# Performance work log

Measured on AMD Instinct MI355X. Metric: run time of the kernel, lower is better.

Reference implementation:

```python
import jax, jax.numpy as jnp
import numpy as np

B, N, K, C = 8, 4096, 16, 128
HID, DEPTH = 4 * C, 2
EPS = 1e-5


def _bn(x, g, b, m, v):
    # BatchNorm1d in eval mode over the last (channel) dim
    return (x - m) * (g * jax.lax.rsqrt(v + EPS)) + b


def _ffn(x, w1, b1, w2, b2, g, bt, m, v):
    h = jax.nn.relu(jnp.einsum('bnc,ch->bnh', x, w1) + b1)
    y = jnp.einsum('bnh,hc->bnc', h, w2) + b2
    return _bn(y, g, bt, m, v)


def setup_inputs() -> dict:
    key = jax.random.key(0)
    ks = jax.random.split(key, 24)
    s = 0.05
    inp = {
        'x': jax.random.normal(ks[0], (B, N, C), jnp.float32),
        'knn_idx': jax.random.randint(ks[1], (B, N, K), 0, N, jnp.int64),
        'mlp0_w1': jax.random.normal(ks[2], (C, HID), jnp.float32) * s,
        'mlp0_b1': jax.random.normal(ks[3], (HID,), jnp.float32) * s,
        'mlp0_w2': jax.random.normal(ks[4], (HID, C), jnp.float32) * s,
        'mlp0_b2': jax.random.normal(ks[5], (C,), jnp.float32) * s,
        'mlp0_g': jax.random.uniform(ks[6], (C,), jnp.float32, 0.5, 1.5),
        'mlp0_beta': jax.random.normal(ks[7], (C,), jnp.float32) * s,
        'mlp0_m': jnp.zeros((C,), jnp.float32),
        'mlp0_v': jnp.ones((C,), jnp.float32),
        'vfr_w': jax.random.normal(ks[8], (DEPTH, C, C), jnp.float32) * s,
        'vfr_b': jax.random.normal(ks[9], (DEPTH, C), jnp.float32) * s,
        'vfr_g': jax.random.uniform(ks[10], (DEPTH, C), jnp.float32, 0.5, 1.5),
        'vfr_beta': jax.random.normal(ks[11], (DEPTH, C), jnp.float32) * s,
        'vfr_m': jnp.zeros((DEPTH, C), jnp.float32),
        'vfr_v': jnp.ones((DEPTH, C), jnp.float32),
        'ffn_w1': jax.random.normal(ks[12], (DEPTH, C, HID), jnp.float32) * s,
        'ffn_b1': jax.random.normal(ks[13], (DEPTH, HID), jnp.float32) * s,
        'ffn_w2': jax.random.normal(ks[14], (DEPTH, HID, C), jnp.float32) * s,
        'ffn_b2': jax.random.normal(ks[15], (DEPTH, C), jnp.float32) * s,
        'ffn_g': jax.random.uniform(ks[16], (DEPTH, C), jnp.float32, 0.5, 1.5),
        'ffn_beta': jax.random.normal(ks[17], (DEPTH, C), jnp.float32) * s,
        'ffn_m': jnp.zeros((DEPTH, C), jnp.float32),
        'ffn_v': jnp.ones((DEPTH, C), jnp.float32),
    }
    return inp


def reference(x, knn_idx,
              mlp0_w1, mlp0_b1, mlp0_w2, mlp0_b2, mlp0_g, mlp0_beta, mlp0_m, mlp0_v,
              vfr_w, vfr_b, vfr_g, vfr_beta, vfr_m, vfr_v,
              ffn_w1, ffn_b1, ffn_w2, ffn_b2, ffn_g, ffn_beta, ffn_m, ffn_v):
    # eval mode: DropPath is identity, BatchNorm uses running stats
    x = x + _ffn(x, mlp0_w1, mlp0_b1, mlp0_w2, mlp0_b2, mlp0_g, mlp0_beta, mlp0_m, mlp0_v)
    gather = jax.vmap(lambda pts, idx: pts[idx])  # [N,C],[N,K] -> [N,K,C]
    for i in range(DEPTH):
        # VFR: linear -> knn gather -> edge diff -> max over K -> BN
        h = jnp.einsum('bnc,cd->bnd', x, vfr_w[i]) + vfr_b[i]
        nb = gather(h, knn_idx)                      # [B,N,K,C]
        agg = jnp.max(nb - h[:, :, None, :], axis=2)  # [B,N,C]
        x = x + _bn(agg, vfr_g[i], vfr_beta[i], vfr_m[i], vfr_v[i])
        x = x + _ffn(x, ffn_w1[i], ffn_b1[i], ffn_w2[i], ffn_b2[i],
                     ffn_g[i], ffn_beta[i], ffn_m[i], ffn_v[i])
    return x
```

## Files before the change

### kernel.cpp

```cpp
#include <hip/hip_runtime.h>
#include <hip/hip_bf16.h>
#include <stdint.h>

typedef __attribute__((ext_vector_type(8))) __bf16 bf16x8;
typedef __attribute__((ext_vector_type(4))) float floatx4;

#define EPS 1e-5f

__device__ __forceinline__ unsigned short f2bf(float f) {
    union { float f; unsigned int u; } x; x.f = f;
    unsigned int r = x.u + 0x7fffu + ((x.u >> 16) & 1u);
    return (unsigned short)(r >> 16);
}
__device__ __forceinline__ float bf2f_lo(unsigned int u) {
    union { unsigned int u; float f; } x; x.u = u << 16; return x.f;
}
__device__ __forceinline__ float bf2f_hi(unsigned int u) {
    union { unsigned int u; float f; } x; x.u = u & 0xffff0000u; return x.f;
}

struct Params {
    const float* x_in;
    const int*   knn;
    const float* w1s[3];
    const float* w2s[3];
    const float* vws[2];
    unsigned short* W1P[3];
    unsigned short* W2P[3];
    unsigned short* VTP[2];
    const float* b1s[3];
    const float* b2s[3];
    const float* gs[3];
    const float* bes[3];
    const float* ms[3];
    const float* vvs[3];
    const float* vbb[2];
    const float* vgg[2];
    const float* vbt[2];
    const float* vmm[2];
    const float* vva[2];
    float* xf;
};

__global__ __launch_bounds__(256) void pack_weights(Params P) {
    const int gtid = blockIdx.x * 256 + threadIdx.x;
    const int GT   = gridDim.x * 256;
#pragma unroll
    for (int t = 0; t < 3; ++t) {
        const float* s1 = P.w1s[t];
        unsigned short* d1 = P.W1P[t];
        for (int idx = gtid; idx < 65536; idx += GT) {
            int h = idx & 511, k = idx >> 9;
            int hf = h >> 8, w = (h >> 5) & 7, mt = (h >> 4) & 1, ln = h & 15;
            int ks = (k >> 5) & 3, q = (k >> 3) & 3, j = k & 7;
            d1[hf * 32768 + w * 4096 + mt * 2048 + ks * 512 + q * 128 + ln * 8 + j]
                = f2bf(s1[idx]);
        }
        const float* s2 = P.w2s[t];
        unsigned short* d2 = P.W2P[t];
        for (int idx = gtid; idx < 65536; idx += GT) {
            int c = idx & 127, h = idx >> 7;
            int hf = h >> 8, ks = (h >> 5) & 7, q = (h >> 3) & 3, j = h & 7;
            int wg = c >> 5, nt = (c >> 4) & 1, ln = c & 15;
            d2[hf * 32768 + wg * 8192 + nt * 4096 + ks * 512 + q * 128 + ln * 8 + j]
                = f2bf(s2[idx]);
        }
    }
#pragma unroll
    for (int t = 0; t < 2; ++t) {
        const float* sv = P.vws[t];
        unsigned short* dv = P.VTP[t];
        for (int idx = gtid; idx < 16384; idx += GT) {
            int c = idx & 127, k = idx >> 7;
            int ks = (k >> 5) & 3, q = (k >> 3) & 3, j = k & 7;
            int wg = c >> 5, nt = (c >> 4) & 1, ln = c & 15;
            dv[wg * 4096 + nt * 2048 + ks * 512 + q * 128 + ln * 8 + j] = f2bf(sv[idx]);
        }
    }
}

template <int LOADX, int TE, int TF, int TV>
__global__ __launch_bounds__(512, 4)
void stage(Params P, const float* __restrict__ xold_g,
           const unsigned short* __restrict__ VbIn,
           unsigned short* __restrict__ VbOut)
{
    __shared__ __align__(16) unsigned short xt[64 * 136];
    __shared__ __align__(16) unsigned short ht[64 * 264];
    const int tid  = threadIdx.x;
    const int lane = tid & 63;
    const int w    = tid >> 6;
    const int q    = lane >> 4;
    const int ln   = lane & 15;
    const int wg   = w & 3;
    const int wh   = w >> 2;
    const int phys = blockIdx.x;
    const int bid  = (phys & 7) * 64 + (phys >> 3);
    const int p0   = bid << 6;
    const floatx4 zero = {0.f, 0.f, 0.f, 0.f};

    if constexpr (LOADX) {
        const int r = tid >> 3, c = tid & 7;
        const float4* src = (const float4*)(xold_g + (size_t)(p0 + r) * 128 + c * 16);
#pragma unroll
        for (int i = 0; i < 2; ++i) {
            float4 a = src[2 * i], b = src[2 * i + 1];
            uint4 pk;
            pk.x = (unsigned int)f2bf(a.x) | ((unsigned int)f2bf(a.y) << 16);
            pk.y = (unsigned int)f2bf(a.z) | ((unsigned int)f2bf(a.w) << 16);
            pk.z = (unsigned int)f2bf(b.x) | ((unsigned int)f2bf(b.y) << 16);
            pk.w = (unsigned int)f2bf(b.z) | ((unsigned int)f2bf(b.w) << 16);
            *(uint4*)&xt[(r * 17 + c * 2 + i) * 8] = pk;
        }
    }

    if constexpr (TE >= 0) {
        const int ch0 = ln * 8;
        float sc[8], of[8];
#pragma unroll
        for (int j2 = 0; j2 < 8; ++j2) {
            float g  = P.vgg[TE][ch0 + j2];
            float bt = P.vbt[TE][ch0 + j2];
            float mu = P.vmm[TE][ch0 + j2];
            float va = P.vva[TE][ch0 + j2];
            sc[j2] = g * rsqrtf(va + EPS);
            of[j2] = bt - mu * sc[j2];
        }
#pragma unroll
        for (int it = 0; it < 2; ++it) {
            const int pl = it * 32 + w * 4 + q;
            const int p  = p0 + pl;
            const int b  = p >> 12;
            uint4 sv = *(const uint4*)(VbIn + (size_t)p * 128 + ch0);
            const int* kp = P.knn + (size_t)p * 16;
            int4 ka = *(const int4*)(kp);
            int4 kb = *(const int4*)(kp + 4);
            int4 kc = *(const int4*)(kp + 8);
            int4 kd = *(const int4*)(kp + 12);
            const unsigned short* vbase = VbIn + (((size_t)b << 12) << 7) + ch0;
            float m[8];
#pragma unroll
            for (int j2 = 0; j2 < 8; ++j2) m[j2] = -3.4e38f;
#define GATH(IDX) { uint4 u4 = *(const uint4*)(vbase + ((size_t)(IDX) << 7));      \
            m[0] = fmaxf(m[0], bf2f_lo(u4.x)); m[1] = fmaxf(m[1], bf2f_hi(u4.x)); \
            m[2] = fmaxf(m[2], bf2f_lo(u4.y)); m[3] = fmaxf(m[3], bf2f_hi(u4.y)); \
            m[4] = fmaxf(m[4], bf2f_lo(u4.z)); m[5] = fmaxf(m[5], bf2f_hi(u4.z)); \
            m[6] = fmaxf(m[6], bf2f_lo(u4.w)); m[7] = fmaxf(m[7], bf2f_hi(u4.w)); }
            GATH(ka.x) GATH(ka.y) GATH(ka.z) GATH(ka.w)
            GATH(kb.x) GATH(kb.y) GATH(kb.z) GATH(kb.w)
            GATH(kc.x) GATH(kc.y) GATH(kc.z) GATH(kc.w)
            GATH(kd.x) GATH(kd.y) GATH(kd.z) GATH(kd.w)
#undef GATH
            const float* xrow = xold_g + (size_t)p * 128 + ch0;
            float4 x0 = *(const float4*)xrow;
            float4 x1 = *(const float4*)(xrow + 4);
            float s_[8];
            s_[0] = bf2f_lo(sv.x); s_[1] = bf2f_hi(sv.x);
            s_[2] = bf2f_lo(sv.y); s_[3] = bf2f_hi(sv.y);
            s_[4] = bf2f_lo(sv.z); s_[5] = bf2f_hi(sv.z);
            s_[6] = bf2f_lo(sv.w); s_[7] = bf2f_hi(sv.w);
            float xo[8] = {x0.x, x0.y, x0.z, x0.w, x1.x, x1.y, x1.z, x1.w};
            unsigned int pw[8];
#pragma unroll
            for (int j2 = 0; j2 < 8; ++j2) {
                float xn = xo[j2] + (m[j2] - s_[j2]) * sc[j2] + of[j2];
                pw[j2] = (unsigned int)f2bf(xn);
            }
            uint4 pk;
            pk.x = pw[0] | (pw[1] << 16);
            pk.y = pw[2] | (pw[3] << 16);
            pk.z = pw[4] | (pw[5] << 16);
            pk.w = pw[6] | (pw[7] << 16);
            *(uint4*)&xt[(pl * 17 + ln) * 8] = pk;
        }
    }
    __syncthreads();

    floatx4 acc2[2][2];
#pragma unroll
    for (int i = 0; i < 2; ++i)
#pragma unroll
        for (int j = 0; j < 2; ++j) acc2[i][j] = zero;

    const unsigned short* W1 = P.W1P[TF];
    const unsigned short* W2 = P.W2P[TF];
    const float* b1 = P.b1s[TF];

#pragma unroll
    for (int hf = 0; hf < 2; ++hf) {
        floatx4 acc1[2][4];
#pragma unroll
        for (int i = 0; i < 2; ++i)
#pragma unroll
            for (int j = 0; j < 4; ++j) acc1[i][j] = zero;
        const unsigned short* a1 = W1 + hf * 32768 + w * 4096 + q * 128 + ln * 8;
#pragma unroll
        for (int ks = 0; ks < 4; ++ks) {
            bf16x8 bfr[4];
#pragma unroll
            for (int nt = 0; nt < 4; ++nt)
                bfr[nt] = *(const bf16x8*)&xt[((16 * nt + ln) * 17 + 4 * ks + q) * 8];
#pragma unroll
            for (int mt = 0; mt < 2; ++mt) {
                bf16x8 af = *(const bf16x8*)(a1 + mt * 2048 + ks * 512);
#pragma unroll
                for (int nt = 0; nt < 4; ++nt)
                    acc1[mt][nt] = __builtin_amdgcn_mfma_f32_16x16x32_bf16(
                        af, bfr[nt], acc1[mt][nt], 0, 0, 0);
            }
        }
        if (hf > 0) __syncthreads();
#pragma unroll
        for (int mt = 0; mt < 2; ++mt) {
            const int hloc = 32 * w + 16 * mt + 4 * q;
            const int gh   = 256 * hf + hloc;
            const float bv0 = b1[gh], bv1 = b1[gh + 1];
            const float bv2 = b1[gh + 2], bv3 = b1[gh + 3];
            const int c16  = hloc >> 3;
            const int half = q & 1;
#pragma unroll
            for (int nt = 0; nt < 4; ++nt) {
                const int pt = 16 * nt + ln;
                float v0 = acc1[mt][nt][0] + bv0; v0 = v0 > 0.f ? v0 : 0.f;
                float v1 = acc1[mt][nt][1] + bv1; v1 = v1 > 0.f ? v1 : 0.f;
                float v2 = acc1[mt][nt][2] + bv2; v2 = v2 > 0.f ? v2 : 0.f;
                float v3 = acc1[mt][nt][3] + bv3; v3 = v3 > 0.f ? v3 : 0.f;
                uint2 pk;
                pk.x = (unsigned int)f2bf(v0) | ((unsigned int)f2bf(v1) << 16);
                pk.y = (unsigned int)f2bf(v2) | ((unsigned int)f2bf(v3) << 16);
                *(uint2*)&ht[(pt * 33 + c16) * 8 + half * 4] = pk;
            }
        }
        __syncthreads();
        const unsigned short* b2b = W2 + hf * 32768 + wg * 8192 + q * 128 + ln * 8;
#pragma unroll
        for (int ks = 0; ks < 8; ++ks) {
            bf16x8 bw[2];
#pragma unroll
            for (int nt = 0; nt < 2; ++nt)
                bw[nt] = *(const bf16x8*)(b2b + nt * 4096 + ks * 512);
#pragma unroll
            for (int mt = 0; mt < 2; ++mt) {
                const int pt = 32 * wh + 16 * mt + ln;
                bf16x8 ah = *(const bf16x8*)&ht[(pt * 33 + 4 * ks + q) * 8];
#pragma unroll
                for (int nt = 0; nt < 2; ++nt)
                    acc2[mt][nt] = __builtin_amdgcn_mfma_f32_16x16x32_bf16(
                        ah, bw[nt], acc2[mt][nt], 0, 0, 0);
            }
        }
    }

    {
        const float* b2   = P.b2s[TF];
        const float* gam  = P.gs[TF];
        const float* bet  = P.bes[TF];
        const float* mean = P.ms[TF];
        const float* var  = P.vvs[TF];
#pragma unroll
        for (int nt = 0; nt < 2; ++nt) {
            const int c = 32 * wg + 16 * nt + ln;
            const float scv = gam[c] * rsqrtf(var[c] + EPS);
            const float off = (b2[c] - mean[c]) * scv + bet[c];
#pragma unroll
            for (int mt = 0; mt < 2; ++mt) {
#pragma unroll
                for (int r = 0; r < 4; ++r) {
                    const int pt = 32 * wh + 16 * mt + 4 * q + r;
                    const int xa = (pt * 17 + (c >> 3)) * 8 + (c & 7);
                    float base = bf2f_lo((unsigned int)xt[xa]);
                    float xn = base + acc2[mt][nt][r] * scv + off;
                    P.xf[(size_t)(p0 + pt) * 128 + c] = xn;
                    if constexpr (TV >= 0) xt[xa] = f2bf(xn);
                }
            }
        }
    }

    if constexpr (TV >= 0) {
        __syncthreads();
        const unsigned short* VT = P.VTP[TV];
        floatx4 acc[2][2];
#pragma unroll
        for (int i = 0; i < 2; ++i)
#pragma unroll
            for (int j = 0; j < 2; ++j) acc[i][j] = zero;
        const unsigned short* bb2 = VT + wg * 4096 + q * 128 + ln * 8;
#pragma unroll
        for (int ks = 0; ks < 4; ++ks) {
            bf16x8 bw[2];
#pragma unroll
            for (int nt = 0; nt < 2; ++nt)
                bw[nt] = *(const bf16x8*)(bb2 + nt * 2048 + ks * 512);
#pragma unroll
            for (int mt = 0; mt < 2; ++mt) {
                const int pt = 32 * wh + 16 * mt + ln;
                bf16x8 ax = *(const bf16x8*)&xt[(pt * 17 + 4 * ks + q) * 8];
#pragma unroll
                for (int nt = 0; nt < 2; ++nt)
                    acc[mt][nt] = __builtin_amdgcn_mfma_f32_16x16x32_bf16(
                        ax, bw[nt], acc[mt][nt], 0, 0, 0);
            }
        }
        const float* vb = P.vbb[TV];
#pragma unroll
        for (int nt = 0; nt < 2; ++nt) {
            const int c = 32 * wg + 16 * nt + ln;
            const float bia = vb[c];
#pragma unroll
            for (int mt = 0; mt < 2; ++mt)
#pragma unroll
                for (int r = 0; r < 4; ++r) {
                    const int pt = 32 * wh + 16 * mt + 4 * q + r;
                    VbOut[(size_t)(p0 + pt) * 128 + c] = f2bf(acc[mt][nt][r] + bia);
                }
        }
    }
}

extern "C" void kernel_launch(void* const* d_in, const int* in_sizes, int n_in,
                              void* d_out, int out_size, void* d_ws, size_t ws_size,
                              hipStream_t stream)
{
    Params p;
    p.x_in = (const float*)d_in[0];
    p.knn  = (const int*)d_in[1];
    const float* w1  = (const float*)d_in[2];
    const float* b1  = (const float*)d_in[3];
    const float* w2  = (const float*)d_in[4];
    const float* b2  = (const float*)d_in[5];
    const float* g0  = (const float*)d_in[6];
    const float* be0 = (const float*)d_in[7];
    const float* m0p = (const float*)d_in[8];
    const float* v0p = (const float*)d_in[9];
    const float* vw  = (const float*)d_in[10];
    const float* vbp = (const float*)d_in[11];
    const float* vgp = (const float*)d_in[12];
    const float* vbe = (const float*)d_in[13];
    const float* vmp = (const float*)d_in[14];
    const float* vvp = (const float*)d_in[15];
    const float* fw1 = (const float*)d_in[16];
    const float* fb1 = (const float*)d_in[17];
    const float* fw2 = (const float*)d_in[18];
    const float* fb2 = (const float*)d_in[19];
    const float* fg  = (const float*)d_in[20];
    const float* fbe = (const float*)d_in[21];
    const float* fm  = (const float*)d_in[22];
    const float* fv  = (const float*)d_in[23];

    p.w1s[0] = w1;  p.w1s[1] = fw1; p.w1s[2] = fw1 + 65536;
    p.w2s[0] = w2;  p.w2s[1] = fw2; p.w2s[2] = fw2 + 65536;
    p.vws[0] = vw;  p.vws[1] = vw + 16384;
    p.b1s[0] = b1;  p.b1s[1] = fb1; p.b1s[2] = fb1 + 512;
    p.b2s[0] = b2;  p.b2s[1] = fb2; p.b2s[2] = fb2 + 128;
    p.gs[0]  = g0;  p.gs[1]  = fg;  p.gs[2]  = fg + 128;
    p.bes[0] = be0; p.bes[1] = fbe; p.bes[2] = fbe + 128;
    p.ms[0]  = m0p; p.ms[1]  = fm;  p.ms[2]  = fm + 128;
    p.vvs[0] = v0p; p.vvs[1] = fv;  p.vvs[2] = fv + 128;
    p.vbb[0] = vbp; p.vbb[1] = vbp + 128;
    p.vgg[0] = vgp; p.vgg[1] = vgp + 128;
    p.vbt[0] = vbe; p.vbt[1] = vbe + 128;
    p.vmm[0] = vmp; p.vmm[1] = vmp + 128;
    p.vva[0] = vvp; p.vva[1] = vvp + 128;

    char* ws = (char*)d_ws;
    unsigned short* Vb0 = (unsigned short*)ws;
    unsigned short* Vb1 = (unsigned short*)(ws + (size_t)(8 << 20));
    unsigned short* u   = (unsigned short*)(ws + (size_t)(16 << 20));
    for (int i = 0; i < 3; ++i) p.W1P[i] = u + i * 65536;
    for (int i = 0; i < 3; ++i) p.W2P[i] = u + 196608 + i * 65536;
    for (int i = 0; i < 2; ++i) p.VTP[i] = u + 393216 + i * 16384;
    p.xf = (float*)d_out;

    pack_weights<<<dim3(512), 256, 0, stream>>>(p);
    stage<1, -1, 0, 0><<<dim3(512), 512, 0, stream>>>(p, p.x_in, nullptr, Vb0);
    stage<0,  0, 1, 1><<<dim3(512), 512, 0, stream>>>(p, p.xf, Vb0, Vb1);
    stage<0,  1, 2, -1><<<dim3(512), 512, 0, stream>>>(p, p.xf, Vb1, nullptr);
}
```

Baseline: 192.3 us.

## Halve point tile to 32, use 256-thread blocks, swizzle LDS, keep residual in fp32

Each block now handles 32 points with 4 waves instead of 64 points with 8 waves, doubling the grid to 1024 blocks. The hidden dimension is processed in four chunks of 128, and the weight packing is reorganized to match. LDS tiles switch from padded rows to XOR-swizzled layouts to avoid bank conflicts in less space. The residual is kept as fp32 in shared memory instead of being re-read from the bf16 tile, which raises accuracy but adds extra syncs and shared-memory traffic. The aim is higher occupancy and parallelism, traded against reduced reuse of each weight fetch per block.

After: 189.0 us. About the same (-1.7%).

```diff
diff --git a/kernel.cpp b/kernel.cpp
--- a/kernel.cpp
+++ b/kernel.cpp
@@ -7,15 +7,15 @@
 
 #define EPS 1e-5f
 
-__device__ __forceinline__ unsigned short f2bf(float f) {
+static __device__ __forceinline__ unsigned short f2bf(float f) {
     union { float f; unsigned int u; } x; x.f = f;
     unsigned int r = x.u + 0x7fffu + ((x.u >> 16) & 1u);
     return (unsigned short)(r >> 16);
 }
-__device__ __forceinline__ float bf2f_lo(unsigned int u) {
+static __device__ __forceinline__ float bf2f_lo(unsigned int u) {
     union { unsigned int u; float f; } x; x.u = u << 16; return x.f;
 }
-__device__ __forceinline__ float bf2f_hi(unsigned int u) {
+static __device__ __forceinline__ float bf2f_hi(unsigned int u) {
     union { unsigned int u; float f; } x; x.u = u & 0xffff0000u; return x.f;
 }
 
@@ -51,18 +51,19 @@
         unsigned short* d1 = P.W1P[t];
         for (int idx = gtid; idx < 65536; idx += GT) {
             int h = idx & 511, k = idx >> 9;
-            int hf = h >> 8, w = (h >> 5) & 7, mt = (h >> 4) & 1, ln = h & 15;
-            int ks = (k >> 5) & 3, q = (k >> 3) & 3, j = k & 7;
-            d1[hf * 32768 + w * 4096 + mt * 2048 + ks * 512 + q * 128 + ln * 8 + j]
+            int hf = h >> 7, w = (h >> 5) & 3, mt = (h >> 4) & 1, ln = h & 15;
+            int ks = k >> 5, q = (k >> 3) & 3, j = k & 7;
+            d1[hf * 16384 + w * 4096 + mt * 2048 + ks * 512 + q * 128 + ln * 8 + j]
                 = f2bf(s1[idx]);
         }
         const float* s2 = P.w2s[t];
         unsigned short* d2 = P.W2P[t];
         for (int idx = gtid; idx < 65536; idx += GT) {
             int c = idx & 127, h = idx >> 7;
-            int hf = h >> 8, ks = (h >> 5) & 7, q = (h >> 3) & 3, j = h & 7;
-            int wg = c >> 5, nt = (c >> 4) & 1, ln = c & 15;
-            d2[hf * 32768 + wg * 8192 + nt * 4096 + ks * 512 + q * 128 + ln * 8 + j]
+            int hf = h >> 7, hk = h & 127;
+            int ks = hk >> 5, q = (hk >> 3) & 3, j = hk & 7;
+            int w = c >> 5, nt = (c >> 4) & 1, ln = c & 15;
+            d2[hf * 16384 + w * 4096 + nt * 2048 + ks * 512 + q * 128 + ln * 8 + j]
                 = f2bf(s2[idx]);
         }
     }
@@ -72,75 +73,85 @@
         unsigned short* dv = P.VTP[t];
         for (int idx = gtid; idx < 16384; idx += GT) {
             int c = idx & 127, k = idx >> 7;
-            int ks = (k >> 5) & 3, q = (k >> 3) & 3, j = k & 7;
-            int wg = c >> 5, nt = (c >> 4) & 1, ln = c & 15;
-            dv[wg * 4096 + nt * 2048 + ks * 512 + q * 128 + ln * 8 + j] = f2bf(sv[idx]);
+            int ks = k >> 5, q = (k >> 3) & 3, j = k & 7;
+            int w = c >> 5, nt = (c >> 4) & 1, ln = c & 15;
+            dv[w * 4096 + nt * 2048 + ks * 512 + q * 128 + ln * 8 + j] = f2bf(sv[idx]);
         }
     }
 }
 
 template <int LOADX, int TE, int TF, int TV>
-__global__ __launch_bounds__(512, 4)
+__global__ __launch_bounds__(256, 4)
 void stage(Params P, const float* __restrict__ xold_g,
            const unsigned short* __restrict__ VbIn,
            unsigned short* __restrict__ VbOut)
 {
-    __shared__ __align__(16) unsigned short xt[64 * 136];
-    __shared__ __align__(16) unsigned short ht[64 * 264];
-    const int tid  = threadIdx.x;
-    const int lane = tid & 63;
-    const int w    = tid >> 6;
-    const int q    = lane >> 4;
-    const int ln   = lane & 15;
-    const int wg   = w & 3;
-    const int wh   = w >> 2;
-    const int phys = blockIdx.x;
-    const int bid  = (phys & 7) * 64 + (phys >> 3);
-    const int p0   = bid << 6;
+    __shared__ __align__(16) unsigned short xt[4096];
+    __shared__ __align__(16) float buf_f[4096];
+    const int tid   = threadIdx.x;
+    const int lane  = tid & 63;
+    const int w     = tid >> 6;
+    const int q     = lane >> 4;
+    const int ln    = lane & 15;
+    const int sw    = ln & 7;
+    const int phys  = blockIdx.x;
+    const int batch = phys & 7;
+    const int blk   = phys >> 3;
+    const int p0    = (batch << 12) + (blk << 5);
     const floatx4 zero = {0.f, 0.f, 0.f, 0.f};
+    uint2* ht2 = (uint2*)buf_f;
 
     if constexpr (LOADX) {
-        const int r = tid >> 3, c = tid & 7;
-        const float4* src = (const float4*)(xold_g + (size_t)(p0 + r) * 128 + c * 16);
+        const int r = tid >> 3, cc = tid & 7;
+        const float4* src = (const float4*)(xold_g + (size_t)(p0 + r) * 128 + cc * 16);
+        float4* dstf = (float4*)&buf_f[r * 128 + cc * 16];
 #pragma unroll
         for (int i = 0; i < 2; ++i) {
             float4 a = src[2 * i], b = src[2 * i + 1];
+            dstf[2 * i]     = a;
+            dstf[2 * i + 1] = b;
+            int kq = cc * 2 + i;
             uint4 pk;
             pk.x = (unsigned int)f2bf(a.x) | ((unsigned int)f2bf(a.y) << 16);
             pk.y = (unsigned int)f2bf(a.z) | ((unsigned int)f2bf(a.w) << 16);
             pk.z = (unsigned int)f2bf(b.x) | ((unsigned int)f2bf(b.y) << 16);
             pk.w = (unsigned int)f2bf(b.z) | ((unsigned int)f2bf(b.w) << 16);
-            *(uint4*)&xt[(r * 17 + c * 2 + i) * 8] = pk;
+            *(uint4*)&xt[(r * 16 + (kq ^ (r & 7))) * 8] = pk;
         }
     }
 
     if constexpr (TE >= 0) {
         const int ch0 = ln * 8;
         float sc[8], of[8];
-#pragma unroll
-        for (int j2 = 0; j2 < 8; ++j2) {
-            float g  = P.vgg[TE][ch0 + j2];
-            float bt = P.vbt[TE][ch0 + j2];
-            float mu = P.vmm[TE][ch0 + j2];
-            float va = P.vva[TE][ch0 + j2];
-            sc[j2] = g * rsqrtf(va + EPS);
-            of[j2] = bt - mu * sc[j2];
+        {
+            float4 ga = *(const float4*)(P.vgg[TE] + ch0), gb = *(const float4*)(P.vgg[TE] + ch0 + 4);
+            float4 ba = *(const float4*)(P.vbt[TE] + ch0), bb = *(const float4*)(P.vbt[TE] + ch0 + 4);
+            float4 ma = *(const float4*)(P.vmm[TE] + ch0), mb = *(const float4*)(P.vmm[TE] + ch0 + 4);
+            float4 va = *(const float4*)(P.vva[TE] + ch0), vb = *(const float4*)(P.vva[TE] + ch0 + 4);
+            const float gv[8] = {ga.x, ga.y, ga.z, ga.w, gb.x, gb.y, gb.z, gb.w};
+            const float bv[8] = {ba.x, ba.y, ba.z, ba.w, bb.x, bb.y, bb.z, bb.w};
+            const float mv[8] = {ma.x, ma.y, ma.z, ma.w, mb.x, mb.y, mb.z, mb.w};
+            const float vvv[8] = {va.x, va.y, va.z, va.w, vb.x, vb.y, vb.z, vb.w};
+#pragma unroll
+            for (int j = 0; j < 8; ++j) {
+                sc[j] = gv[j] * rsqrtf(vvv[j] + EPS);
+                of[j] = bv[j] - mv[j] * sc[j];
+            }
         }
 #pragma unroll
         for (int it = 0; it < 2; ++it) {
-            const int pl = it * 32 + w * 4 + q;
+            const int pl = it * 16 + w * 4 + q;
             const int p  = p0 + pl;
-            const int b  = p >> 12;
             uint4 sv = *(const uint4*)(VbIn + (size_t)p * 128 + ch0);
             const int* kp = P.knn + (size_t)p * 16;
             int4 ka = *(const int4*)(kp);
             int4 kb = *(const int4*)(kp + 4);
             int4 kc = *(const int4*)(kp + 8);
             int4 kd = *(const int4*)(kp + 12);
-            const unsigned short* vbase = VbIn + (((size_t)b << 12) << 7) + ch0;
+            const unsigned short* vbase = VbIn + ((size_t)batch << 19) + ch0;
             float m[8];
 #pragma unroll
-            for (int j2 = 0; j2 < 8; ++j2) m[j2] = -3.4e38f;
+            for (int j = 0; j < 8; ++j) m[j] = -3.4e38f;
 #define GATH(IDX) { uint4 u4 = *(const uint4*)(vbase + ((size_t)(IDX) << 7));      \
             m[0] = fmaxf(m[0], bf2f_lo(u4.x)); m[1] = fmaxf(m[1], bf2f_hi(u4.x)); \
             m[2] = fmaxf(m[2], bf2f_lo(u4.y)); m[3] = fmaxf(m[3], bf2f_hi(u4.y)); \
@@ -151,29 +162,42 @@
             GATH(kc.x) GATH(kc.y) GATH(kc.z) GATH(kc.w)
             GATH(kd.x) GATH(kd.y) GATH(kd.z) GATH(kd.w)
 #undef GATH
-            const float* xrow = xold_g + (size_t)p * 128 + ch0;
-            float4 x0 = *(const float4*)xrow;
-            float4 x1 = *(const float4*)(xrow + 4);
             float s_[8];
             s_[0] = bf2f_lo(sv.x); s_[1] = bf2f_hi(sv.x);
             s_[2] = bf2f_lo(sv.y); s_[3] = bf2f_hi(sv.y);
             s_[4] = bf2f_lo(sv.z); s_[5] = bf2f_hi(sv.z);
             s_[6] = bf2f_lo(sv.w); s_[7] = bf2f_hi(sv.w);
+            const float* xrow = xold_g + (size_t)p * 128 + ch0;
+            float4 x0 = *(const float4*)xrow;
+            float4 x1 = *(const float4*)(xrow + 4);
             float xo[8] = {x0.x, x0.y, x0.z, x0.w, x1.x, x1.y, x1.z, x1.w};
+            float xn[8];
             unsigned int pw[8];
 #pragma unroll
-            for (int j2 = 0; j2 < 8; ++j2) {
-                float xn = xo[j2] + (m[j2] - s_[j2]) * sc[j2] + of[j2];
-                pw[j2] = (unsigned int)f2bf(xn);
-            }
+            for (int j = 0; j < 8; ++j) {
+                xn[j] = xo[j] + (m[j] - s_[j]) * sc[j] + of[j];
+                pw[j] = (unsigned int)f2bf(xn[j]);
+            }
+            *(float4*)&buf_f[pl * 128 + ch0]     = make_float4(xn[0], xn[1], xn[2], xn[3]);
+            *(float4*)&buf_f[pl * 128 + ch0 + 4] = make_float4(xn[4], xn[5], xn[6], xn[7]);
             uint4 pk;
             pk.x = pw[0] | (pw[1] << 16);
             pk.y = pw[2] | (pw[3] << 16);
             pk.z = pw[4] | (pw[5] << 16);
             pk.w = pw[6] | (pw[7] << 16);
-            *(uint4*)&xt[(pl * 17 + ln) * 8] = pk;
-        }
-    }
+            *(uint4*)&xt[(pl * 16 + (ln ^ (pl & 7))) * 8] = pk;
+        }
+    }
+    __syncthreads();
+
+    float xr[2][2][4];
+#pragma unroll
+    for (int mt = 0; mt < 2; ++mt)
+#pragma unroll
+        for (int nt = 0; nt < 2; ++nt)
+#pragma unroll
+            for (int r = 0; r < 4; ++r)
+                xr[mt][nt][r] = buf_f[(16 * mt + 4 * q + r) * 128 + 32 * w + 16 * nt + ln];
     __syncthreads();
 
     floatx4 acc2[2][2];
@@ -187,39 +211,38 @@
     const float* b1 = P.b1s[TF];
 
 #pragma unroll
-    for (int hf = 0; hf < 2; ++hf) {
-        floatx4 acc1[2][4];
+    for (int hf = 0; hf < 4; ++hf) {
+        floatx4 acc1[2][2];
 #pragma unroll
         for (int i = 0; i < 2; ++i)
 #pragma unroll
-            for (int j = 0; j < 4; ++j) acc1[i][j] = zero;
-        const unsigned short* a1 = W1 + hf * 32768 + w * 4096 + q * 128 + ln * 8;
+            for (int j = 0; j < 2; ++j) acc1[i][j] = zero;
+        const unsigned short* a1 = W1 + hf * 16384 + w * 4096 + q * 128 + ln * 8;
 #pragma unroll
         for (int ks = 0; ks < 4; ++ks) {
-            bf16x8 bfr[4];
-#pragma unroll
-            for (int nt = 0; nt < 4; ++nt)
-                bfr[nt] = *(const bf16x8*)&xt[((16 * nt + ln) * 17 + 4 * ks + q) * 8];
+            bf16x8 bfr[2];
+#pragma unroll
+            for (int nt = 0; nt < 2; ++nt)
+                bfr[nt] = *(const bf16x8*)&xt[((16 * nt + ln) * 16 + ((4 * ks + q) ^ sw)) * 8];
 #pragma unroll
             for (int mt = 0; mt < 2; ++mt) {
                 bf16x8 af = *(const bf16x8*)(a1 + mt * 2048 + ks * 512);
 #pragma unroll
-                for (int nt = 0; nt < 4; ++nt)
+                for (int nt = 0; nt < 2; ++nt)
                     acc1[mt][nt] = __builtin_amdgcn_mfma_f32_16x16x32_bf16(
                         af, bfr[nt], acc1[mt][nt], 0, 0, 0);
             }
         }
-        if (hf > 0) __syncthreads();
 #pragma unroll
         for (int mt = 0; mt < 2; ++mt) {
             const int hloc = 32 * w + 16 * mt + 4 * q;
-            const int gh   = 256 * hf + hloc;
+            const int gh   = 128 * hf + hloc;
             const float bv0 = b1[gh], bv1 = b1[gh + 1];
             const float bv2 = b1[gh + 2], bv3 = b1[gh + 3];
             const int c16  = hloc >> 3;
             const int half = q & 1;
 #pragma unroll
-            for (int nt = 0; nt < 4; ++nt) {
+            for (int nt = 0; nt < 2; ++nt) {
                 const int pt = 16 * nt + ln;
                 float v0 = acc1[mt][nt][0] + bv0; v0 = v0 > 0.f ? v0 : 0.f;
                 float v1 = acc1[mt][nt][1] + bv1; v1 = v1 > 0.f ? v1 : 0.f;
@@ -228,27 +251,28 @@
                 uint2 pk;
                 pk.x = (unsigned int)f2bf(v0) | ((unsigned int)f2bf(v1) << 16);
                 pk.y = (unsigned int)f2bf(v2) | ((unsigned int)f2bf(v3) << 16);
-                *(uint2*)&ht[(pt * 33 + c16) * 8 + half * 4] = pk;
+                ht2[(pt * 16 + (c16 ^ (pt & 7))) * 2 + half] = pk;
             }
         }
         __syncthreads();
-        const unsigned short* b2b = W2 + hf * 32768 + wg * 8192 + q * 128 + ln * 8;
-#pragma unroll
-        for (int ks = 0; ks < 8; ++ks) {
+        const unsigned short* b2b = W2 + hf * 16384 + w * 4096 + q * 128 + ln * 8;
+#pragma unroll
+        for (int ks = 0; ks < 4; ++ks) {
             bf16x8 bw[2];
 #pragma unroll
             for (int nt = 0; nt < 2; ++nt)
-                bw[nt] = *(const bf16x8*)(b2b + nt * 4096 + ks * 512);
+                bw[nt] = *(const bf16x8*)(b2b + nt * 2048 + ks * 512);
 #pragma unroll
             for (int mt = 0; mt < 2; ++mt) {
-                const int pt = 32 * wh + 16 * mt + ln;
-                bf16x8 ah = *(const bf16x8*)&ht[(pt * 33 + 4 * ks + q) * 8];
+                const int pt = 16 * mt + ln;
+                bf16x8 ah = *(const bf16x8*)&ht2[(pt * 16 + ((4 * ks + q) ^ (pt & 7))) * 2];
 #pragma unroll
                 for (int nt = 0; nt < 2; ++nt)
                     acc2[mt][nt] = __builtin_amdgcn_mfma_f32_16x16x32_bf16(
                         ah, bw[nt], acc2[mt][nt], 0, 0, 0);
             }
         }
+        __syncthreads();
     }
 
     {
@@ -259,19 +283,18 @@
         const float* var  = P.vvs[TF];
 #pragma unroll
         for (int nt = 0; nt < 2; ++nt) {
-            const int c = 32 * wg + 16 * nt + ln;
+            const int c = 32 * w + 16 * nt + ln;
             const float scv = gam[c] * rsqrtf(var[c] + EPS);
             const float off = (b2[c] - mean[c]) * scv + bet[c];
 #pragma unroll
             for (int mt = 0; mt < 2; ++mt) {
 #pragma unroll
                 for (int r = 0; r < 4; ++r) {
-                    const int pt = 32 * wh + 16 * mt + 4 * q + r;
-                    const int xa = (pt * 17 + (c >> 3)) * 8 + (c & 7);
-                    float base = bf2f_lo((unsigned int)xt[xa]);
-                    float xn = base + acc2[mt][nt][r] * scv + off;
+                    const int pt = 16 * mt + 4 * q + r;
+                    float xn = xr[mt][nt][r] + acc2[mt][nt][r] * scv + off;
                     P.xf[(size_t)(p0 + pt) * 128 + c] = xn;
-                    if constexpr (TV >= 0) xt[xa] = f2bf(xn);
+                    if constexpr (TV >= 0)
+                        xt[(pt * 16 + ((c >> 3) ^ (pt & 7))) * 8 + (c & 7)] = f2bf(xn);
                 }
             }
         }
@@ -285,7 +308,7 @@
         for (int i = 0; i < 2; ++i)
 #pragma unroll
             for (int j = 0; j < 2; ++j) acc[i][j] = zero;
-        const unsigned short* bb2 = VT + wg * 4096 + q * 128 + ln * 8;
+        const unsigned short* bb2 = VT + w * 4096 + q * 128 + ln * 8;
 #pragma unroll
         for (int ks = 0; ks < 4; ++ks) {
             bf16x8 bw[2];
@@ -294,8 +317,7 @@
                 bw[nt] = *(const bf16x8*)(bb2 + nt * 2048 + ks * 512);
 #pragma unroll
             for (int mt = 0; mt < 2; ++mt) {
-                const int pt = 32 * wh + 16 * mt + ln;
-                bf16x8 ax = *(const bf16x8*)&xt[(pt * 17 + 4 * ks + q) * 8];
+                bf16x8 ax = *(const bf16x8*)&xt[((16 * mt + ln) * 16 + ((4 * ks + q) ^ sw)) * 8];
 #pragma unroll
                 for (int nt = 0; nt < 2; ++nt)
                     acc[mt][nt] = __builtin_amdgcn_mfma_f32_16x16x32_bf16(
@@ -305,13 +327,13 @@
         const float* vb = P.vbb[TV];
 #pragma unroll
         for (int nt = 0; nt < 2; ++nt) {
-            const int c = 32 * wg + 16 * nt + ln;
+            const int c = 32 * w + 16 * nt + ln;
             const float bia = vb[c];
 #pragma unroll
             for (int mt = 0; mt < 2; ++mt)
 #pragma unroll
                 for (int r = 0; r < 4; ++r) {
-                    const int pt = 32 * wh + 16 * mt + 4 * q + r;
+                    const int pt = 16 * mt + 4 * q + r;
                     VbOut[(size_t)(p0 + pt) * 128 + c] = f2bf(acc[mt][nt][r] + bia);
                 }
         }
@@ -373,7 +395,7 @@
     p.xf = (float*)d_out;
 
     pack_weights<<<dim3(512), 256, 0, stream>>>(p);
-    stage<1, -1, 0, 0><<<dim3(512), 512, 0, stream>>>(p, p.x_in, nullptr, Vb0);
-    stage<0,  0, 1, 1><<<dim3(512), 512, 0, stream>>>(p, p.xf, Vb0, Vb1);
-    stage<0,  1, 2, -1><<<dim3(512), 512, 0, stream>>>(p, p.xf, Vb1, nullptr);
-}
+    stage<1, -1, 0, 0><<<dim3(1024), 256, 0, stream>>>(p, p.x_in, nullptr, Vb0);
+    stage<0,  0, 1, 1><<<dim3(1024), 256, 0, stream>>>(p, p.xf, Vb0, Vb1);
+    stage<0,  1, 2, -1><<<dim3(1024), 256, 0, stream>>>(p, p.xf, Vb1, nullptr);
+}
```
